# Performance work log

Measured on AMD Instinct MI355X. Metric: run time of the kernel, lower is better.

Reference implementation:

```python
import jax, jax.numpy as jnp
import numpy as np
import math

L = 2      # n_layers
D = 1024   # d_model
H = 16     # n_heads
DH = D // H
DFF = 4 * D
B = 2
T = 2048
AV = 64    # action_vocab
OV = 4096  # obs_vocab


def setup_inputs() -> dict:
    key = jax.random.key(0)
    ks = iter(jax.random.split(key, 40))
    def n(shape, s=0.02):
        return jax.random.normal(next(ks), shape, dtype=jnp.float32) * s
    inp = {}
    inp['actions'] = jax.random.randint(next(ks), (B, T), 0, AV)
    inp['observations'] = jax.random.randint(next(ks), (B, T), 0, OV)
    inp['action_emb'] = n((AV, D))
    inp['obs_emb'] = n((OV, D))
    inp['type_emb'] = n((2, D))
    inp['Wq'] = n((L, D, D)); inp['bq'] = jnp.zeros((L, D), jnp.float32)
    inp['Wk'] = n((L, D, D)); inp['bk'] = jnp.zeros((L, D), jnp.float32)
    inp['Wv'] = n((L, D, D)); inp['bv'] = jnp.zeros((L, D), jnp.float32)
    inp['Wo'] = n((L, D, D)); inp['bo'] = jnp.zeros((L, D), jnp.float32)
    inp['ln1_g'] = jnp.ones((L, D), jnp.float32); inp['ln1_b'] = jnp.zeros((L, D), jnp.float32)
    inp['ln2_g'] = jnp.ones((L, D), jnp.float32); inp['ln2_b'] = jnp.zeros((L, D), jnp.float32)
    inp['W1'] = n((L, D, DFF)); inp['b1'] = jnp.zeros((L, DFF), jnp.float32)
    inp['W2'] = n((L, DFF, D)); inp['b2'] = jnp.zeros((L, D), jnp.float32)
    inp['out_g'] = jnp.ones((D,), jnp.float32); inp['out_b'] = jnp.zeros((D,), jnp.float32)
    inp['Wout'] = n((D, OV)); inp['bout'] = jnp.zeros((OV,), jnp.float32)
    return inp


def _ln(x, g, b, eps=1e-5):
    m = x.mean(-1, keepdims=True)
    v = ((x - m) ** 2).mean(-1, keepdims=True)
    return (x - m) / jnp.sqrt(v + eps) * g + b


def reference(actions, observations, action_emb, obs_emb, type_emb,
              Wq, bq, Wk, bk, Wv, bv, Wo, bo,
              ln1_g, ln1_b, ln2_g, ln2_b, W1, b1, W2, b2,
              out_g, out_b, Wout, bout):
    Bsz, Tl = actions.shape
    # token-type 0 for actions, 1 for observations; summed embeddings
    x = (action_emb[actions] + type_emb[0]) + (obs_emb[observations] + type_emb[1])

    # interleaved RoPE tables: freqs[t, j] = t * base**(-2j/d_head)
    inv_freq = 1.0 / (10000.0 ** (jnp.arange(0, DH, 2, dtype=jnp.float32) / DH))
    freqs = jnp.outer(jnp.arange(Tl, dtype=jnp.float32), inv_freq)  # (T, DH//2)
    cos, sin = jnp.cos(freqs), jnp.sin(freqs)

    def rope(z):  # z: (B, H, T, DH) with even/odd interleaving
        z1, z2 = z[..., 0::2], z[..., 1::2]
        o1 = z1 * cos - z2 * sin
        o2 = z1 * sin + z2 * cos
        return jnp.stack([o1, o2], axis=-1).reshape(z.shape)

    causal = jnp.triu(jnp.ones((Tl, Tl), dtype=bool), k=1)  # True above diagonal
    scale = math.sqrt(DH)

    for i in range(L):
        h = _ln(x, ln1_g[i], ln1_b[i])
        Q = (h @ Wq[i] + bq[i]).reshape(Bsz, Tl, H, DH).transpose(0, 2, 1, 3)
        K = (h @ Wk[i] + bk[i]).reshape(Bsz, Tl, H, DH).transpose(0, 2, 1, 3)
        V = (h @ Wv[i] + bv[i]).reshape(Bsz, Tl, H, DH).transpose(0, 2, 1, 3)
        Q, K = rope(Q), rope(K)
        scores = jnp.einsum('bhqd,bhkd->bhqk', Q, K) / scale
        scores = jnp.where(causal, -jnp.inf, scores)
        attn = jax.nn.softmax(scores, axis=-1)
        o = jnp.einsum('bhqk,bhkd->bhqd', attn, V)
        o = o.transpose(0, 2, 1, 3).reshape(Bsz, Tl, D)
        x = x + (o @ Wo[i] + bo[i])
        h2 = _ln(x, ln2_g[i], ln2_b[i])
        ff = jax.nn.gelu(h2 @ W1[i] + b1[i], approximate=False) @ W2[i] + b2[i]
        x = x + ff

    x = _ln(x, out_g, out_b)
    return x @ Wout + bout
```

## Files before the change

### kernel.cpp

```cpp
#include <hip/hip_runtime.h>
#include <hip/hip_bf16.h>
#include <cstdint>

typedef __bf16 bf16;
typedef __attribute__((ext_vector_type(8))) __bf16 bf16x8;
typedef __attribute__((ext_vector_type(4))) float f32x4;

#define LYR 2
#define DIM 1024
#define NH 16
#define DHD 64
#define DFF 4096
#define BB 2
#define TT 2048
#define NTOK (BB*TT)
#define OVS 4096

#define ROPE_L2 0.41524101186092029f

__device__ __forceinline__ float ldw(const void* p, size_t i, int isbf) {
    return isbf ? (float)((const bf16*)p)[i] : ((const float*)p)[i];
}

__device__ __forceinline__ void gl16(const bf16* g, bf16* l) {
    __builtin_amdgcn_global_load_lds(
        (const __attribute__((address_space(1))) void*)g,
        (__attribute__((address_space(3))) void*)l, 16, 0, 0);
}

__global__ void k_sniff(const unsigned short* __restrict__ g, int* __restrict__ flag) {
    if (threadIdx.x == 0) *flag = (g[0] == 0x3F80u) ? 1 : 0;
}

__global__ void k_embed(const int* __restrict__ act, const int* __restrict__ obs,
                        const void* __restrict__ aemb, const void* __restrict__ oemb,
                        const void* __restrict__ temb, float* __restrict__ x,
                        const int* __restrict__ dflag)
{
    const int isbf = *dflag;
    int i = blockIdx.x;
    int a = act[i], o = obs[i];
    for (int c = threadIdx.x; c < DIM; c += 256)
        x[(size_t)i*DIM + c] = ldw(aemb, (size_t)a*DIM + c, isbf)
                             + ldw(temb, c, isbf)
                             + ldw(oemb, (size_t)o*DIM + c, isbf)
                             + ldw(temb, DIM + c, isbf);
}

__global__ __launch_bounds__(256) void k_ln(const float* __restrict__ x,
    const void* __restrict__ g, const void* __restrict__ b, size_t gOff,
    bf16* __restrict__ out, const int* __restrict__ dflag)
{
    const int isbf = *dflag;
    int row = blockIdx.x, tid = threadIdx.x;
    const float* xr = x + (size_t)row * DIM;
    float4 xv = ((const float4*)xr)[tid];
    float s  = xv.x + xv.y + xv.z + xv.w;
    float s2 = xv.x*xv.x + xv.y*xv.y + xv.z*xv.z + xv.w*xv.w;
#pragma unroll
    for (int off = 32; off > 0; off >>= 1) {
        s  += __shfl_down(s, off);
        s2 += __shfl_down(s2, off);
    }
    __shared__ float rs[4], rq[4];
    if ((tid & 63) == 0) { rs[tid>>6] = s; rq[tid>>6] = s2; }
    __syncthreads();
    float S  = rs[0]+rs[1]+rs[2]+rs[3];
    float Q2 = rq[0]+rq[1]+rq[2]+rq[3];
    float mean = S * (1.f/DIM);
    float var  = Q2 * (1.f/DIM) - mean*mean;
    float rstd = rsqrtf(var + 1e-5f);
    int c = tid*4;
    bf16* po = out + (size_t)row*DIM + c;
    po[0] = (bf16)((xv.x-mean)*rstd*ldw(g,gOff+c,  isbf) + ldw(b,gOff+c,  isbf));
    po[1] = (bf16)((xv.y-mean)*rstd*ldw(g,gOff+c+1,isbf) + ldw(b,gOff+c+1,isbf));
    po[2] = (bf16)((xv.z-mean)*rstd*ldw(g,gOff+c+2,isbf) + ldw(b,gOff+c+2,isbf));
    po[3] = (bf16)((xv.w-mean)*rstd*ldw(g,gOff+c+3,isbf) + ldw(b,gOff+c+3,isbf));
}

__global__ __launch_bounds__(256) void k_cvtT(const void* __restrict__ W, size_t wOff,
    bf16* __restrict__ WT, int K, int N, const int* __restrict__ dflag)
{
    const int isbf = *dflag;
    __shared__ bf16 Ts[64][65];
    const int n0 = blockIdx.x * 64, k0 = blockIdx.y * 64;
    const int t = threadIdx.x;
    const int cn = t & 63, rk = t >> 6;
#pragma unroll
    for (int r = 0; r < 16; r++) {
        int kk = rk + r*4;
        Ts[kk][cn] = (bf16)ldw(W, wOff + (size_t)(k0+kk)*N + n0 + cn, isbf);
    }
    __syncthreads();
#pragma unroll
    for (int r = 0; r < 16; r++) {
        int nn = rk + r*4;
        WT[(size_t)(n0+nn)*K + k0 + cn] = Ts[cn][nn];
    }
}

template<int MODE, int BN = 128>
__global__ __launch_bounds__(256) void k_gemm(const bf16* __restrict__ A,
    const bf16* __restrict__ BT,
    const void* __restrict__ bias, const void* __restrict__ bias2,
    const void* __restrict__ bias3, size_t biasOff,
    const float* __restrict__ res, void* __restrict__ out, int K, int N,
    const int* __restrict__ dflag)
{
    const int isbf = *dflag;
    constexpr int NI = BN / 32;
    __shared__ __align__(16) bf16 As[4][128*32];
    __shared__ __align__(16) bf16 Bs[4][BN*32];
    const int tid = threadIdx.x;
    const int m0 = blockIdx.x * 128, n0 = blockIdx.y * BN;
    const int w = tid >> 6, lane = tid & 63;
    const int wr = (w >> 1) * 64, wc = (w & 1) * (BN/2);
    const int lm = lane & 15, kg = lane >> 4;

    const int srow = lane >> 2, sk = (lane & 3) * 8;
    const bf16* aG = A  + (size_t)(m0 + w*32 + srow)*K + sk;
    const bf16* bG = BT + (size_t)(n0 + w*(BN/4) + srow)*K + sk;
    const int r0 = w*32, r1 = w*32 + 16;
    const int rb0 = w*(BN/4), rb1 = w*(BN/4) + 16;

    const int nt = K >> 5;

    auto STAGE = [&](int buf, int t) {
        const int kb = t << 5;
        gl16(aG + kb,                 &As[buf][r0*32]);
        gl16(aG + (size_t)16*K + kb,  &As[buf][r1*32]);
        gl16(bG + kb,                 &Bs[buf][rb0*32]);
        if constexpr (BN == 128)
            gl16(bG + (size_t)16*K + kb, &Bs[buf][rb1*32]);
    };

    STAGE(0, 0);
    STAGE(1, 1 < nt ? 1 : 0);
    STAGE(2, 2 < nt ? 2 : 0);

    f32x4 acc[4][NI] = {};

    for (int t = 0; t < nt; ++t) {
        if constexpr (BN == 128)
            asm volatile("s_waitcnt vmcnt(8)" ::: "memory");
        else
            asm volatile("s_waitcnt vmcnt(6)" ::: "memory");
        __builtin_amdgcn_s_barrier();
        {
            int tn = (t + 3 < nt) ? t + 3 : nt - 1;
            STAGE((t + 3) & 3, tn);
        }
        const bf16* as = &As[t & 3][0];
        const bf16* bs = &Bs[t & 3][0];
        bf16x8 af[4], bfr[NI];
#pragma unroll
        for (int i = 0; i < 4; i++)
            af[i]  = *(const bf16x8*)&as[(wr + i*16 + lm)*32 + kg*8];
#pragma unroll
        for (int i = 0; i < NI; i++)
            bfr[i] = *(const bf16x8*)&bs[(wc + i*16 + lm)*32 + kg*8];
#pragma unroll
        for (int mi = 0; mi < 4; mi++)
#pragma unroll
            for (int ni = 0; ni < NI; ni++)
                acc[mi][ni] = __builtin_amdgcn_mfma_f32_16x16x32_bf16(af[mi], bfr[ni], acc[mi][ni], 0, 0, 0);
    }
    asm volatile("s_waitcnt vmcnt(0)" ::: "memory");

#pragma unroll
    for (int mi = 0; mi < 4; mi++) {
#pragma unroll
        for (int ni = 0; ni < NI; ni++) {
            int col = n0 + wc + ni*16 + lm;
            int which = col >> 10;
            const void* bp = bias;
            int bcol = col;
            if (MODE == 7) {
                bcol = col & 1023;
                if (which == 1) bp = bias2; else if (which == 2) bp = bias3;
            }
            float bv = ldw(bp, biasOff + bcol, isbf);
#pragma unroll
            for (int r = 0; r < 4; r++) {
                int row = m0 + wr + mi*16 + kg*4 + r;
                float val = acc[mi][ni][r] + bv;
                if (MODE == 1) {
                    size_t o = (size_t)row * N + col;
                    if (isbf) ((bf16*)out)[o] = (bf16)val;
                    else      ((float*)out)[o] = val;
                } else if (MODE == 2) {
                    size_t o = (size_t)row * N + col;
                    ((float*)out)[o] = res[o] + val;
                } else if (MODE == 3) {
                    float gl = 0.5f * val * (1.f + erff(val * 0.70710678118654752f));
                    ((bf16*)out)[(size_t)row * N + col] = (bf16)gl;
                } else {
                    float part = __shfl_xor(val, 1);
                    int cc = col & 1023;
                    int h = cc >> 6, d = cc & 63;
                    int bidx = row >> 11, t = row & (TT - 1);
                    float o;
                    if (which == 2) {
                        o = val;
                    } else {
                        float fi = (float)(d >> 1);
                        float freq = (float)t * exp2f(-fi * ROPE_L2);
                        float sn, cs; sincosf(freq, &sn, &cs);
                        o = val * cs + part * ((d & 1) ? sn : -sn);
                        if (which == 0) o *= 0.125f;
                    }
                    size_t oo = (size_t)which * (size_t)(4*1024*1024)
                              + ((size_t)(bidx*NH + h)*TT + t)*DHD + d;
                    ((bf16*)out)[oo] = (bf16)o;
                }
            }
        }
    }
}

#define SK 72
__global__ __launch_bounds__(256) void k_flash(const bf16* __restrict__ q,
    const bf16* __restrict__ k, const bf16* __restrict__ v, bf16* __restrict__ o)
{
    __shared__ __align__(16) bf16 Ks[64*SK];
    __shared__ __align__(16) bf16 Vt[64*SK];
    __shared__ __align__(16) bf16 Pls[4*32*SK];
    const int qb = (TT/128 - 1) - blockIdx.x;
    const int h = blockIdx.y, b = blockIdx.z;
    const int tid = threadIdx.x;
    const int w = tid >> 6, lane = tid & 63;
    const int ln = lane & 15, kg = lane >> 4;
    const size_t bh = ((size_t)(b*NH + h)) * TT;
    const int q0a = qb*128 + w*16;
    const int q0b = q0a + 64;

    const bf16* qpa = q + (bh + q0a + ln)*DHD;
    const bf16* qpb = q + (bh + q0b + ln)*DHD;
    const bf16x8 qf0a = *(const bf16x8*)(qpa + kg*8);
    const bf16x8 qf1a = *(const bf16x8*)(qpa + 32 + kg*8);
    const bf16x8 qf0b = *(const bf16x8*)(qpb + kg*8);
    const bf16x8 qf1b = *(const bf16x8*)(qpb + 32 + kg*8);

    f32x4 oaccA[4] = {}, oaccB[4] = {};
    float mrowA[4] = {-1e30f,-1e30f,-1e30f,-1e30f};
    float mrowB[4] = {-1e30f,-1e30f,-1e30f,-1e30f};
    float lrowA[4] = {0.f,0.f,0.f,0.f};
    float lrowB[4] = {0.f,0.f,0.f,0.f};

    const int sKey = tid >> 2, sDh = (tid & 3) * 16;
    const int vKey = tid & 63, vDh = (tid >> 6) * 16;

    bf16* pwA = &Pls[(w*32)*SK];
    bf16* pwB = &Pls[(w*32 + 16)*SK];

    auto ISSUE = [&](int kt, uint4& k0, uint4& k1, uint4& v0, uint4& v1) {
        const bf16* kp = k + (bh + (size_t)kt*64)*DHD;
        const bf16* vp = v + (bh + (size_t)kt*64)*DHD;
        k0 = *(const uint4*)(kp + sKey*DHD + sDh);
        k1 = *(const uint4*)(kp + sKey*DHD + sDh + 8);
        v0 = *(const uint4*)(vp + vKey*DHD + vDh);
        v1 = *(const uint4*)(vp + vKey*DHD + vDh + 8);
    };
    auto WRITE = [&](const uint4& k0, const uint4& k1, const uint4& v0, const uint4& v1) {
        *(uint4*)&Ks[sKey*SK + sDh]     = k0;
        *(uint4*)&Ks[sKey*SK + sDh + 8] = k1;
        const bf16* p0 = (const bf16*)&v0;
        const bf16* p1 = (const bf16*)&v1;
#pragma unroll
        for (int j = 0; j < 8; j++) {
            Vt[(vDh + j)*SK + vKey]     = p0[j];
            Vt[(vDh + 8 + j)*SK + vKey] = p1[j];
        }
    };

    auto COMPUTE = [&](int kt) {
        const bool doA = (kt <= 2*qb);
        const bool maskA = (kt == 2*qb);
        const bool maskB = (kt == 2*qb + 1);

        f32x4 sa[4], sb[4];
        __builtin_amdgcn_s_setprio(1);
#pragma unroll
        for (int c = 0; c < 4; c++) {
            bf16x8 kf0 = *(const bf16x8*)&Ks[(c*16 + ln)*SK + kg*8];
            bf16x8 kf1 = *(const bf16x8*)&Ks[(c*16 + ln)*SK + 32 + kg*8];
            if (doA) {
                f32x4 z = {};
                z = __builtin_amdgcn_mfma_f32_16x16x32_bf16(qf0a, kf0, z, 0, 0, 0);
                z = __builtin_amdgcn_mfma_f32_16x16x32_bf16(qf1a, kf1, z, 0, 0, 0);
                sa[c] = z;
            }
            f32x4 z = {};
            z = __builtin_amdgcn_mfma_f32_16x16x32_bf16(qf0b, kf0, z, 0, 0, 0);
            z = __builtin_amdgcn_mfma_f32_16x16x32_bf16(qf1b, kf1, z, 0, 0, 0);
            sb[c] = z;
        }
        __builtin_amdgcn_s_setprio(0);
        if (!doA) {
#pragma unroll
            for (int c = 0; c < 4; c++)
#pragma unroll
                for (int r = 0; r < 4; r++) sa[c][r] = -1e30f;
        }

        if (maskA) {
#pragma unroll
            for (int c = 0; c < 4; c++) {
                int key = kt*64 + c*16 + ln;
#pragma unroll
                for (int r = 0; r < 4; r++)
                    if (key > q0a + kg*4 + r) sa[c][r] = -1e30f;
            }
        }
        if (maskB) {
#pragma unroll
            for (int c = 0; c < 4; c++) {
                int key = kt*64 + c*16 + ln;
#pragma unroll
                for (int r = 0; r < 4; r++)
                    if (key > q0b + kg*4 + r) sb[c][r] = -1e30f;
            }
        }

        float corrA[4], corrB[4];
#pragma unroll
        for (int r = 0; r < 4; r++) {
            float ma = fmaxf(fmaxf(sa[0][r], sa[1][r]), fmaxf(sa[2][r], sa[3][r]));
            float mb = fmaxf(fmaxf(sb[0][r], sb[1][r]), fmaxf(sb[2][r], sb[3][r]));
#pragma unroll
            for (int off = 1; off < 16; off <<= 1) {
                ma = fmaxf(ma, __shfl_xor(ma, off));
                mb = fmaxf(mb, __shfl_xor(mb, off));
            }
            float mnA = fmaxf(mrowA[r], ma);
            float mnB = fmaxf(mrowB[r], mb);
            corrA[r] = __expf(mrowA[r] - mnA);
            corrB[r] = __expf(mrowB[r] - mnB);
            mrowA[r] = mnA; mrowB[r] = mnB;
            float rsA = 0.f, rsB = 0.f;
#pragma unroll
            for (int c = 0; c < 4; c++) {
                float pa = __expf(sa[c][r] - mnA);
                float pb = __expf(sb[c][r] - mnB);
                sa[c][r] = pa; sb[c][r] = pb;
                rsA += pa; rsB += pb;
            }
#pragma unroll
            for (int off = 1; off < 16; off <<= 1) {
                rsA += __shfl_xor(rsA, off);
                rsB += __shfl_xor(rsB, off);
            }
            lrowA[r] = lrowA[r]*corrA[r] + rsA;
            lrowB[r] = lrowB[r]*corrB[r] + rsB;
        }
#pragma unroll
        for (int n = 0; n < 4; n++)
#pragma unroll
            for (int r = 0; r < 4; r++) {
                if (doA) oaccA[n][r] *= corrA[r];
                oaccB[n][r] *= corrB[r];
            }

        if (doA) {
#pragma unroll
            for (int c = 0; c < 4; c++)
#pragma unroll
                for (int r = 0; r < 4; r++)
                    pwA[(kg*4 + r)*SK + c*16 + ln] = (bf16)sa[c][r];
        }
#pragma unroll
        for (int c = 0; c < 4; c++)
#pragma unroll
            for (int r = 0; r < 4; r++)
                pwB[(kg*4 + r)*SK + c*16 + ln] = (bf16)sb[c][r];
        bf16x8 pfa0, pfa1;
        if (doA) {
            pfa0 = *(const bf16x8*)&pwA[ln*SK + kg*8];
            pfa1 = *(const bf16x8*)&pwA[ln*SK + 32 + kg*8];
        }
        bf16x8 pfb0 = *(const bf16x8*)&pwB[ln*SK + kg*8];
        bf16x8 pfb1 = *(const bf16x8*)&pwB[ln*SK + 32 + kg*8];

        __builtin_amdgcn_s_setprio(1);
#pragma unroll
        for (int n = 0; n < 4; n++) {
            bf16x8 vf0 = *(const bf16x8*)&Vt[(n*16 + ln)*SK + kg*8];
            bf16x8 vf1 = *(const bf16x8*)&Vt[(n*16 + ln)*SK + 32 + kg*8];
            if (doA) {
                oaccA[n] = __builtin_amdgcn_mfma_f32_16x16x32_bf16(pfa0, vf0, oaccA[n], 0, 0, 0);
                oaccA[n] = __builtin_amdgcn_mfma_f32_16x16x32_bf16(pfa1, vf1, oaccA[n], 0, 0, 0);
            }
            oaccB[n] = __builtin_amdgcn_mfma_f32_16x16x32_bf16(pfb0, vf0, oaccB[n], 0, 0, 0);
            oaccB[n] = __builtin_amdgcn_mfma_f32_16x16x32_bf16(pfb1, vf1, oaccB[n], 0, 0, 0);
        }
        __builtin_amdgcn_s_setprio(0);
    };

    const int nk = 2*qb + 2;
    uint4 ka0, ka1, va0, va1, kb0, kb1, vb0, vb1;
    ISSUE(0, ka0, ka1, va0, va1);
    for (int kt = 0; kt < nk; kt += 2) {
        __syncthreads();
        WRITE(ka0, ka1, va0, va1);
        ISSUE(kt + 1, kb0, kb1, vb0, vb1);
        __syncthreads();
        COMPUTE(kt);
        __syncthreads();
        WRITE(kb0, kb1, vb0, vb1);
        if (kt + 2 < nk) ISSUE(kt + 2, ka0, ka1, va0, va1);
        __syncthreads();
        COMPUTE(kt + 1);
    }

    float invA[4], invB[4];
#pragma unroll
    for (int r = 0; r < 4; r++) { invA[r] = 1.f / lrowA[r]; invB[r] = 1.f / lrowB[r]; }
#pragma unroll
    for (int n = 0; n < 4; n++)
#pragma unroll
        for (int r = 0; r < 4; r++) {
            int ta = q0a + kg*4 + r;
            int tb = q0b + kg*4 + r;
            o[((size_t)(b*TT + ta))*DIM + h*DHD + n*16 + ln] = (bf16)(oaccA[n][r] * invA[r]);
            o[((size_t)(b*TT + tb))*DIM + h*DHD + n*16 + ln] = (bf16)(oaccB[n][r] * invB[r]);
        }
}

extern "C" void kernel_launch(void* const* d_in, const int* in_sizes, int n_in,
                              void* d_out, int out_size, void* d_ws, size_t ws_size,
                              hipStream_t stream)
{
    const int*  actions      = (const int*)d_in[0];
    const int*  observations = (const int*)d_in[1];
    const void* action_emb = d_in[2];
    const void* obs_emb    = d_in[3];
    const void* type_emb   = d_in[4];
    const void* Wq  = d_in[5];
    const void* bq  = d_in[6];
    const void* Wk  = d_in[7];
    const void* bk  = d_in[8];
    const void* Wv  = d_in[9];
    const void* bv  = d_in[10];
    const void* Wo  = d_in[11];
    const void* bo  = d_in[12];
    const void* ln1_g = d_in[13];
    const void* ln1_b = d_in[14];
    const void* ln2_g = d_in[15];
    const void* ln2_b = d_in[16];
    const void* W1  = d_in[17];
    const void* b1  = d_in[18];
    const void* W2  = d_in[19];
    const void* b2  = d_in[20];
    const void* out_g = d_in[21];
    const void* out_b = d_in[22];
    const void* Wout  = d_in[23];
    const void* bout  = d_in[24];

    char* ws = (char*)d_ws;
    const size_t MB = 1024*1024;
    float* xF   = (float*)(ws);
    bf16*  hB   = (bf16*)(ws + 16*MB);
    int*   dflag = (int*)(ws + 24*MB);
    bf16*  qB = (bf16*)d_out;
    bf16*  kB = (bf16*)((char*)d_out + 8*MB);
    bf16*  vB = (bf16*)((char*)d_out + 16*MB);
    bf16*  gB = (bf16*)d_out;
    char*  wt = ((size_t)out_size >= 56*MB) ? ((char*)d_out + 32*MB)
                                            : (ws + 25*MB);
    bf16* WqT = (bf16*)(wt);
    bf16* WkT = (bf16*)(wt + 2*MB);
    bf16* WvT = (bf16*)(wt + 4*MB);
    bf16* WoT = (bf16*)(wt + 6*MB);
    bf16* W1T = (bf16*)(wt + 8*MB);
    bf16* W2T = (bf16*)(wt + 16*MB);
    bf16* WoutT = (bf16*)xF;

    k_sniff<<<1, 64, 0, stream>>>((const unsigned short*)ln1_g, dflag);
    k_embed<<<NTOK, 256, 0, stream>>>(actions, observations, action_emb, obs_emb, type_emb, xF, dflag);
    for (int l = 0; l < LYR; l++) {
        const size_t wo = (size_t)l*DIM*DIM;
        const size_t vo = (size_t)l*DIM;
        k_cvtT<<<dim3(DIM/64, DIM/64), 256, 0, stream>>>(Wq, wo, WqT, DIM, DIM, dflag);
        k_cvtT<<<dim3(DIM/64, DIM/64), 256, 0, stream>>>(Wk, wo, WkT, DIM, DIM, dflag);
        k_cvtT<<<dim3(DIM/64, DIM/64), 256, 0, stream>>>(Wv, wo, WvT, DIM, DIM, dflag);
        k_cvtT<<<dim3(DIM/64, DIM/64), 256, 0, stream>>>(Wo, wo, WoT, DIM, DIM, dflag);
        k_cvtT<<<dim3(DFF/64, DIM/64), 256, 0, stream>>>(W1, (size_t)l*DIM*DFF, W1T, DIM, DFF, dflag);
        k_cvtT<<<dim3(DIM/64, DFF/64), 256, 0, stream>>>(W2, (size_t)l*DFF*DIM, W2T, DFF, DIM, dflag);

        k_ln<<<NTOK, 256, 0, stream>>>(xF, ln1_g, ln1_b, vo, hB, dflag);
        k_gemm<7,128><<<dim3(NTOK/128, 3*DIM/128), 256, 0, stream>>>(hB, WqT, bq, bk, bv, vo, nullptr, qB, DIM, 3*DIM, dflag);
        k_flash<<<dim3(TT/128, NH, BB), 256, 0, stream>>>(qB, kB, vB, hB);
        k_gemm<2,64><<<dim3(NTOK/128, DIM/64), 256, 0, stream>>>(hB, WoT, bo, nullptr, nullptr, vo, xF, xF, DIM, DIM, dflag);
        k_ln<<<NTOK, 256, 0, stream>>>(xF, ln2_g, ln2_b, vo, hB, dflag);
        k_gemm<3,128><<<dim3(NTOK/128, DFF/128), 256, 0, stream>>>(hB, W1T, b1, nullptr, nullptr, (size_t)l*DFF, nullptr, gB, DIM, DFF, dflag);
        k_gemm<2,64><<<dim3(NTOK/128, DIM/64), 256, 0, stream>>>(gB, W2T, b2, nullptr, nullptr, vo, xF, xF, DFF, DIM, dflag);
    }
    k_ln<<<NTOK, 256, 0, stream>>>(xF, out_g, out_b, 0, hB, dflag);
    k_cvtT<<<dim3(OVS/64, DIM/64), 256, 0, stream>>>(Wout, 0, WoutT, DIM, OVS, dflag);
    k_gemm<1,128><<<dim3(NTOK/128, OVS/128), 256, 0, stream>>>(hB, WoutT, bout, nullptr, nullptr, 0, nullptr, d_out, DIM, OVS, dflag);
}
```

Baseline: 1.167 ms.

## Batch weight transposes, split-K W2 GEMM with atomics, double-buffer flash K/V

Three separate changes. The six per-layer weight transpose launches become one kernel with a flat 3072-block grid. The FFN down-projection becomes a split-K GEMM over 4 K-slices that add into the residual buffer with float atomics, which quadruples the grid for the long K=4096 reduction. Flash attention double-buffers K/V in shared memory so each tile is written while the previous one is computed, halving the barriers per tile. The atomics make the summation order non-deterministic and add extra global traffic.

```diff
diff --git a/kernel.cpp b/kernel.cpp
--- a/kernel.cpp
+++ b/kernel.cpp
@@ -78,12 +78,10 @@
     po[3] = (bf16)((xv.w-mean)*rstd*ldw(g,gOff+c+3,isbf) + ldw(b,gOff+c+3,isbf));
 }
 
-__global__ __launch_bounds__(256) void k_cvtT(const void* __restrict__ W, size_t wOff,
-    bf16* __restrict__ WT, int K, int N, const int* __restrict__ dflag)
-{
-    const int isbf = *dflag;
+__device__ __forceinline__ void cvt_tile(const void* __restrict__ W, size_t wOff,
+    bf16* __restrict__ WT, int K, int N, int n0, int k0, int isbf)
+{
     __shared__ bf16 Ts[64][65];
-    const int n0 = blockIdx.x * 64, k0 = blockIdx.y * 64;
     const int t = threadIdx.x;
     const int cn = t & 63, rk = t >> 6;
 #pragma unroll
@@ -96,6 +94,35 @@
     for (int r = 0; r < 16; r++) {
         int nn = rk + r*4;
         WT[(size_t)(n0+nn)*K + k0 + cn] = Ts[cn][nn];
+    }
+}
+
+__global__ __launch_bounds__(256) void k_cvtT(const void* __restrict__ W, size_t wOff,
+    bf16* __restrict__ WT, int K, int N, const int* __restrict__ dflag)
+{
+    cvt_tile(W, wOff, WT, K, N, blockIdx.x * 64, blockIdx.y * 64, *dflag);
+}
+
+__global__ __launch_bounds__(256) void k_cvt6(const void* __restrict__ Wq,
+    const void* __restrict__ Wk, const void* __restrict__ Wv, const void* __restrict__ Wo,
+    const void* __restrict__ W1, const void* __restrict__ W2,
+    size_t woD, size_t woF, bf16* __restrict__ wt, const int* __restrict__ dflag)
+{
+    const int isbf = *dflag;
+    const int bid = blockIdx.x;
+    if (bid < 1024) {
+        const int job = bid >> 8, local = bid & 255;
+        const void* src = (job == 0) ? Wq : (job == 1) ? Wk : (job == 2) ? Wv : Wo;
+        bf16* dst = wt + (size_t)job * (DIM*DIM);
+        cvt_tile(src, woD, dst, DIM, DIM, (local & 15)*64, (local >> 4)*64, isbf);
+    } else if (bid < 2048) {
+        const int local = bid - 1024;
+        bf16* dst = wt + (size_t)4*(DIM*DIM);
+        cvt_tile(W1, woF, dst, DIM, DFF, (local & 63)*64, (local >> 6)*64, isbf);
+    } else {
+        const int local = bid - 2048;
+        bf16* dst = wt + (size_t)4*(DIM*DIM) + (size_t)DIM*DFF;
+        cvt_tile(W2, woF, dst, DFF, DIM, (local & 15)*64, (local >> 4)*64, isbf);
     }
 }
 
@@ -117,13 +144,16 @@
     const int wr = (w >> 1) * 64, wc = (w & 1) * (BN/2);
     const int lm = lane & 15, kg = lane >> 4;
 
+    int Keff = K, kOff = 0;
+    if (MODE == 8) { int KS = K / gridDim.z; kOff = blockIdx.z * KS; Keff = KS; }
+
     const int srow = lane >> 2, sk = (lane & 3) * 8;
-    const bf16* aG = A  + (size_t)(m0 + w*32 + srow)*K + sk;
-    const bf16* bG = BT + (size_t)(n0 + w*(BN/4) + srow)*K + sk;
+    const bf16* aG = A  + (size_t)(m0 + w*32 + srow)*K + sk + kOff;
+    const bf16* bG = BT + (size_t)(n0 + w*(BN/4) + srow)*K + sk + kOff;
     const int r0 = w*32, r1 = w*32 + 16;
     const int rb0 = w*(BN/4), rb1 = w*(BN/4) + 16;
 
-    const int nt = K >> 5;
+    const int nt = Keff >> 5;
 
     auto STAGE = [&](int buf, int t) {
         const int kb = t << 5;
@@ -180,6 +210,7 @@
                 if (which == 1) bp = bias2; else if (which == 2) bp = bias3;
             }
             float bv = ldw(bp, biasOff + bcol, isbf);
+            if (MODE == 8 && blockIdx.z != 0) bv = 0.f;
 #pragma unroll
             for (int r = 0; r < 4; r++) {
                 int row = m0 + wr + mi*16 + kg*4 + r;
@@ -191,6 +222,8 @@
                 } else if (MODE == 2) {
                     size_t o = (size_t)row * N + col;
                     ((float*)out)[o] = res[o] + val;
+                } else if (MODE == 8) {
+                    unsafeAtomicAdd(&((float*)out)[(size_t)row * N + col], val);
                 } else if (MODE == 3) {
                     float gl = 0.5f * val * (1.f + erff(val * 0.70710678118654752f));
                     ((bf16*)out)[(size_t)row * N + col] = (bf16)gl;
@@ -222,8 +255,8 @@
 __global__ __launch_bounds__(256) void k_flash(const bf16* __restrict__ q,
     const bf16* __restrict__ k, const bf16* __restrict__ v, bf16* __restrict__ o)
 {
-    __shared__ __align__(16) bf16 Ks[64*SK];
-    __shared__ __align__(16) bf16 Vt[64*SK];
+    __shared__ __align__(16) bf16 Ks0[64*SK], Ks1[64*SK];
+    __shared__ __align__(16) bf16 Vt0[64*SK], Vt1[64*SK];
     __shared__ __align__(16) bf16 Pls[4*32*SK];
     const int qb = (TT/128 - 1) - blockIdx.x;
     const int h = blockIdx.y, b = blockIdx.z;
@@ -261,7 +294,8 @@
         v0 = *(const uint4*)(vp + vKey*DHD + vDh);
         v1 = *(const uint4*)(vp + vKey*DHD + vDh + 8);
     };
-    auto WRITE = [&](const uint4& k0, const uint4& k1, const uint4& v0, const uint4& v1) {
+    auto WRITE = [&](bf16* Ks, bf16* Vt, const uint4& k0, const uint4& k1,
+                     const uint4& v0, const uint4& v1) {
         *(uint4*)&Ks[sKey*SK + sDh]     = k0;
         *(uint4*)&Ks[sKey*SK + sDh + 8] = k1;
         const bf16* p0 = (const bf16*)&v0;
@@ -273,7 +307,7 @@
         }
     };
 
-    auto COMPUTE = [&](int kt) {
+    auto COMPUTE = [&](int kt, const bf16* Ks, const bf16* Vt) {
         const bool doA = (kt <= 2*qb);
         const bool maskA = (kt == 2*qb);
         const bool maskB = (kt == 2*qb + 1);
@@ -399,17 +433,18 @@
     const int nk = 2*qb + 2;
     uint4 ka0, ka1, va0, va1, kb0, kb1, vb0, vb1;
     ISSUE(0, ka0, ka1, va0, va1);
+    WRITE(Ks0, Vt0, ka0, ka1, va0, va1);
+    ISSUE(1, kb0, kb1, vb0, vb1);
+    __syncthreads();
     for (int kt = 0; kt < nk; kt += 2) {
+        COMPUTE(kt, Ks0, Vt0);
+        if (kt + 2 < nk) ISSUE(kt + 2, ka0, ka1, va0, va1);
+        WRITE(Ks1, Vt1, kb0, kb1, vb0, vb1);
         __syncthreads();
-        WRITE(ka0, ka1, va0, va1);
-        ISSUE(kt + 1, kb0, kb1, vb0, vb1);
+        COMPUTE(kt + 1, Ks1, Vt1);
+        if (kt + 3 < nk) ISSUE(kt + 3, kb0, kb1, vb0, vb1);
+        if (kt + 2 < nk) WRITE(Ks0, Vt0, ka0, ka1, va0, va1);
         __syncthreads();
-        COMPUTE(kt);
-        __syncthreads();
-        WRITE(kb0, kb1, vb0, vb1);
-        if (kt + 2 < nk) ISSUE(kt + 2, ka0, ka1, va0, va1);
-        __syncthreads();
-        COMPUTE(kt + 1);
     }
 
     float invA[4], invB[4];
@@ -467,25 +502,20 @@
     bf16*  gB = (bf16*)d_out;
     char*  wt = ((size_t)out_size >= 56*MB) ? ((char*)d_out + 32*MB)
                                             : (ws + 25*MB);
-    bf16* WqT = (bf16*)(wt);
-    bf16* WkT = (bf16*)(wt + 2*MB);
-    bf16* WvT = (bf16*)(wt + 4*MB);
-    bf16* WoT = (bf16*)(wt + 6*MB);
-    bf16* W1T = (bf16*)(wt + 8*MB);
-    bf16* W2T = (bf16*)(wt + 16*MB);
+    bf16* wtB = (bf16*)wt;
+    bf16* WqT = wtB;
+    bf16* WoT = wtB + (size_t)3*DIM*DIM;
+    bf16* W1T = wtB + (size_t)4*DIM*DIM;
+    bf16* W2T = wtB + (size_t)4*DIM*DIM + (size_t)DIM*DFF;
     bf16* WoutT = (bf16*)xF;
 
     k_sniff<<<1, 64, 0, stream>>>((const unsigned short*)ln1_g, dflag);
     k_embed<<<NTOK, 256, 0, stream>>>(actions, observations, action_emb, obs_emb, type_emb, xF, dflag);
     for (int l = 0; l < LYR; l++) {
         const size_t wo = (size_t)l*DIM*DIM;
+        const size_t woF = (size_t)l*DIM*DFF;
         const size_t vo = (size_t)l*DIM;
-        k_cvtT<<<dim3(DIM/64, DIM/64), 256, 0, stream>>>(Wq, wo, WqT, DIM, DIM, dflag);
-        k_cvtT<<<dim3(DIM/64, DIM/64), 256, 0, stream>>>(Wk, wo, WkT, DIM, DIM, dflag);
-        k_cvtT<<<dim3(DIM/64, DIM/64), 256, 0, stream>>>(Wv, wo, WvT, DIM, DIM, dflag);
-        k_cvtT<<<dim3(DIM/64, DIM/64), 256, 0, stream>>>(Wo, wo, WoT, DIM, DIM, dflag);
-        k_cvtT<<<dim3(DFF/64, DIM/64), 256, 0, stream>>>(W1, (size_t)l*DIM*DFF, W1T, DIM, DFF, dflag);
-        k_cvtT<<<dim3(DIM/64, DFF/64), 256, 0, stream>>>(W2, (size_t)l*DFF*DIM, W2T, DFF, DIM, dflag);
+        k_cvt6<<<3072, 256, 0, stream>>>(Wq, Wk, Wv, Wo, W1, W2, wo, woF, wtB, dflag);
 
         k_ln<<<NTOK, 256, 0, stream>>>(xF, ln1_g, ln1_b, vo, hB, dflag);
         k_gemm<7,128><<<dim3(NTOK/128, 3*DIM/128), 256, 0, stream>>>(hB, WqT, bq, bk, bv, vo, nullptr, qB, DIM, 3*DIM, dflag);
@@ -493,7 +523,7 @@
         k_gemm<2,64><<<dim3(NTOK/128, DIM/64), 256, 0, stream>>>(hB, WoT, bo, nullptr, nullptr, vo, xF, xF, DIM, DIM, dflag);
         k_ln<<<NTOK, 256, 0, stream>>>(xF, ln2_g, ln2_b, vo, hB, dflag);
         k_gemm<3,128><<<dim3(NTOK/128, DFF/128), 256, 0, stream>>>(hB, W1T, b1, nullptr, nullptr, (size_t)l*DFF, nullptr, gB, DIM, DFF, dflag);
-        k_gemm<2,64><<<dim3(NTOK/128, DIM/64), 256, 0, stream>>>(gB, W2T, b2, nullptr, nullptr, vo, xF, xF, DFF, DIM, dflag);
+        k_gemm<8,64><<<dim3(NTOK/128, DIM/64, 4), 256, 0, stream>>>(gB, W2T, b2, nullptr, nullptr, vo, nullptr, xF, DFF, DIM, dflag);
     }
     k_ln<<<NTOK, 256, 0, stream>>>(xF, out_g, out_b, 0, hB, dflag);
     k_cvtT<<<dim3(OVS/64, DIM/64), 256, 0, stream>>>(Wout, 0, WoutT, DIM, OVS, dflag);
```

After: 1.451 ms. 1.24x slower.
